# Performance work log

Hardware: AMD Instinct MI355X
Metric: run time of the kernel (lower is better)

The kernel has to match this reference:

```python
import math
import jax, jax.numpy as jnp
import numpy as np

T, D, H, HD, ETA, R = 4096, 1024, 8, 64, 4, 7
EPS = 1e-5


def _discounted_sum(start_state, x, discounts):
    """state[t] = state[t-1]*discounts[t] + x[t], scanned over leading axis T."""
    def step(s, xd):
        xt, dt = xd
        s = s * dt + xt
        return s, s
    _, ys = jax.lax.scan(step, start_state, (x, discounts))
    return ys  # (T, *)


def _forward(inputs, terminations, tilde_k_prev, tilde_v_prev, s_prev, tick,
             W_kqv, b_kqv, W_p, b_p, W_proj, b_proj):
    cur_seq = inputs.shape[0]
    term = terminations.astype(inputs.dtype)

    kqv = (inputs @ W_kqv + b_kqv).reshape(cur_seq, H, 5 * HD)
    keys, queries, values, beta, gammas = jnp.split(kqv, 5, axis=-1)  # each (T,H,HD)
    p = (inputs @ W_p + b_p).reshape(cur_seq, H, 3 * ETA)
    p1, p2, p3 = jnp.split(p, 3, axis=-1)  # each (T,H,ETA)

    # feature-map expansion: outer product over (eta, head_dim) -> flatten to eta*HD
    keys = jnp.einsum('chd,chn->chnd', jax.nn.relu(keys), jax.nn.relu(p1)).reshape(cur_seq, H, ETA * HD)
    queries = jnp.einsum('chd,chn->chnd', jax.nn.relu(queries), jax.nn.relu(p2)).reshape(cur_seq, H, ETA * HD)
    gammas = jnp.einsum('chd,chn->chnd', jax.nn.sigmoid(gammas), jax.nn.sigmoid(p3)).reshape(cur_seq, H, ETA * HD)
    beta = jax.nn.sigmoid(beta)  # (T,H,HD)

    ticks = tick.reshape(1, 1) + jnp.arange(1, cur_seq + 1, dtype=inputs.dtype).reshape(-1, 1)  # (T,1)->(T,R)
    omegas = jnp.linspace(-math.pi, math.pi, R).astype(inputs.dtype).reshape(1, -1)
    occil = jnp.cos(ticks * omegas)  # (T,R)

    values = values * beta
    values = values[:, None, :, :] * occil[:, :, None, None]  # (T,R,H,HD)
    keys = keys * gammas
    s = keys  # (T,H,ETA*HD)
    keys = keys[:, None, :, :] * occil[:, :, None, None]  # (T,R,H,ETA*HD)

    not_term = (1.0 - term).reshape(cur_seq, 1, 1)
    discount_gamma = (1.0 - gammas) * not_term  # (T,H,ETA*HD)
    discount_beta = (1.0 - beta) * not_term     # (T,H,HD)

    final_keys = _discounted_sum(tilde_k_prev, keys, discount_gamma[:, None])    # (T,R,H,ETA*HD)
    final_values = _discounted_sum(tilde_v_prev, values, discount_beta[:, None])  # (T,R,H,HD)
    final_s = _discounted_sum(s_prev, s, discount_gamma)                          # (T,H,ETA*HD)

    kdq = jnp.einsum('crhd,chd->crh', final_keys, queries)
    kv = jnp.einsum('crhd,crh->chd', final_values, kdq)  # sum over r
    norm = jnp.einsum('chd,chd->ch', final_s, queries)
    attn_out = kv / (2 * R * norm[..., None] + EPS)
    attn_out = attn_out.reshape(cur_seq, H * HD) @ W_proj + b_proj  # dropout p=0.0 is identity

    new_tick = tick + cur_seq
    return attn_out, final_keys[-1], final_values[-1], final_s[-1], new_tick


def setup_inputs() -> dict:
    key = jax.random.key(0)
    ks = jax.random.split(key, 5)
    return {
        'inputs': jax.random.normal(ks[0], (T, D), jnp.float32),
        'terminations': jax.random.randint(ks[1], (T,), 0, 2, jnp.int32),
        'tilde_k_prev': jnp.zeros((R, H, ETA * HD), jnp.float32),
        'tilde_v_prev': jnp.zeros((R, H, HD), jnp.float32),
        's_prev': jnp.zeros((H, ETA * HD), jnp.float32),
        'tick': jnp.ones((1,), jnp.float32),
        'W_kqv': jax.random.normal(ks[2], (D, H * HD * 5), jnp.float32) * 0.02,
        'b_kqv': jnp.zeros((H * HD * 5,), jnp.float32),
        'W_p': jax.random.normal(ks[3], (D, H * ETA * 3), jnp.float32) * 0.02,
        'b_p': jnp.zeros((H * ETA * 3,), jnp.float32),
        'W_proj': jax.random.normal(ks[4], (H * HD, D), jnp.float32) * 0.02,
        'b_proj': jnp.zeros((D,), jnp.float32),
    }


def reference(inputs, terminations, tilde_k_prev, tilde_v_prev, s_prev, tick,
              W_kqv, b_kqv, W_p, b_p, W_proj, b_proj):
    return _forward(inputs, terminations, tilde_k_prev, tilde_v_prev, s_prev, tick,
                    W_kqv, b_kqv, W_p, b_p, W_proj, b_proj)
```

## Files before the change

### kernel.cpp

```cpp
#include <hip/hip_runtime.h>
#include <hip/hip_bf16.h>
#include <math.h>

#define T_SEQ 4096
#define DIM   1024
#define NH    8
#define HDIM  64
#define ETA   4
#define NR    7
#define NKQVC 2688
#define CHUNK 16
#define NCHUNK 256

typedef __attribute__((ext_vector_type(8))) short bf16x8;
typedef __attribute__((ext_vector_type(4))) short short4v;
typedef __attribute__((ext_vector_type(4))) float f32x4;

#define KQVC_OFF    0ul
#define OCC_OFF     5505024ul
#define BTPROJ_OFF  5537792ul
#define ATTNBF_OFF  5799936ul
#define BIASC_OFF   6848512ul
#define ABF_OFF     6851328ul
#define BTCAT_OFF   8948480ul
#define YSUM_OFF    6851328ul
#define GBUF_OFF    12618496ul

#define O_ATTN 0ul
#define O_FK   4194304ul
#define O_FV   4208640ul
#define O_FS   4212224ul
#define O_TICK 4214272ul

__device__ __forceinline__ float sigm(float x) { return 1.f / (1.f + __expf(-x)); }

__device__ __forceinline__ short f2bf(float f) {
  union { __hip_bfloat16 b; short s; } u;
  u.b = __float2bfloat16(f);
  return u.s;
}
__device__ __forceinline__ float bf2f(short s) {
  union { __hip_bfloat16 b; short s2; } u;
  u.s2 = s;
  return __bfloat162float(u.b);
}

__device__ __forceinline__ void gload16(const void* g, void* l) {
  __builtin_amdgcn_global_load_lds(
      (const __attribute__((address_space(1))) void*)g,
      (__attribute__((address_space(3))) void*)l, 16, 0, 0);
}

__global__ __launch_bounds__(256) void cast_f32_bf16(
    const float* __restrict__ x, short* __restrict__ y) {
  size_t i = (size_t)(blockIdx.x * 256 + threadIdx.x) * 4;
  float4 v = *(const float4*)(x + i);
  short4v o;
  o.x = f2bf(v.x); o.y = f2bf(v.y); o.z = f2bf(v.z); o.w = f2bf(v.w);
  *(short4v*)(y + i) = o;
}

__global__ __launch_bounds__(256) void transpose_cast(
    const float* __restrict__ W, short* __restrict__ Bt, int K, int N) {
  __shared__ float tile[32][33];
  int n0 = blockIdx.x * 32, k0 = blockIdx.y * 32;
  int tx = threadIdx.x, ty = threadIdx.y;
  for (int i = ty; i < 32; i += 8)
    tile[i][tx] = W[(size_t)(k0 + i) * N + n0 + tx];
  __syncthreads();
  for (int i = ty; i < 32; i += 8)
    Bt[(size_t)(n0 + i) * K + k0 + tx] = f2bf(tile[tx][i]);
}

__global__ __launch_bounds__(256) void concat_bias(
    const float* __restrict__ b_kqv, const float* __restrict__ b_p,
    float* __restrict__ bc) {
  int i = blockIdx.x * 256 + threadIdx.x;
  if (i >= NKQVC) return;
  bc[i] = (i < 2560) ? b_kqv[i] : (i < 2656 ? b_p[i - 2560] : 0.f);
}

template <int OUT_BF16>
__global__ __launch_bounds__(256) void gemm_bt_mfma(
    const short* __restrict__ A, const short* __restrict__ Bt,
    const float* __restrict__ bias, void* __restrict__ Cout,
    int M, int N, int K) {
  __shared__ __align__(16) short lds[16384];

  int nwg = gridDim.x;
  int cpx = nwg >> 3;
  int bid = blockIdx.x;
  int swz = (bid & 7) * cpx + (bid >> 3);
  int nbx = N >> 7;
  int bm0 = (swz / nbx) << 7;
  int bn0 = (swz % nbx) << 7;

  const int tid = threadIdx.x;
  const int w = tid >> 6, l = tid & 63;
  const int wm = w >> 1, wn = w & 1;
  const int fr = l & 15;
  const int fq = l >> 4;

  const int ca = w * 2;
  const short* Ag0 = A + (size_t)(bm0 + ca * 16 + (l >> 2)) * K + (l & 3) * 8;
  const short* Ag1 = Ag0 + (size_t)16 * K;
  const short* Bg0 = Bt + (size_t)(bn0 + ca * 16 + (l >> 2)) * K + (l & 3) * 8;
  const short* Bg1 = Bg0 + (size_t)16 * K;

  f32x4 acc[4][4];
#pragma unroll
  for (int mi = 0; mi < 4; ++mi)
#pragma unroll
    for (int ni = 0; ni < 4; ++ni)
#pragma unroll
      for (int r = 0; r < 4; ++r) acc[mi][ni][r] = 0.f;

  const int KT = K >> 5;
  int cur = 0;
  {
    short* la = &lds[ca * 512];
    short* lb = &lds[4096 + ca * 512];
    gload16(Ag0, la);
    gload16(Ag1, la + 512);
    gload16(Bg0, lb);
    gload16(Bg1, lb + 512);
  }
  __syncthreads();

  for (int kt = 0; kt < KT; ++kt) {
    if (kt + 1 < KT) {
      int nb = (cur ^ 1) * 8192;
      int ko = (kt + 1) * 32;
      short* la = &lds[nb + ca * 512];
      short* lb = &lds[nb + 4096 + ca * 512];
      gload16(Ag0 + ko, la);
      gload16(Ag1 + ko, la + 512);
      gload16(Bg0 + ko, lb);
      gload16(Bg1 + ko, lb + 512);
    }
    const short* ArP = &lds[cur * 8192 + (wm * 64 + fr) * 32 + fq * 8];
    const short* BrP = &lds[cur * 8192 + 4096 + (wn * 64 + fr) * 32 + fq * 8];
    bf16x8 af[4], bfv[4];
#pragma unroll
    for (int mi = 0; mi < 4; ++mi) af[mi] = *(const bf16x8*)(ArP + mi * 512);
#pragma unroll
    for (int ni = 0; ni < 4; ++ni) bfv[ni] = *(const bf16x8*)(BrP + ni * 512);
#pragma unroll
    for (int mi = 0; mi < 4; ++mi)
#pragma unroll
      for (int ni = 0; ni < 4; ++ni)
        acc[mi][ni] = __builtin_amdgcn_mfma_f32_16x16x32_bf16(
            af[mi], bfv[ni], acc[mi][ni], 0, 0, 0);
    __syncthreads();
    cur ^= 1;
  }

  if (OUT_BF16) {
#pragma unroll
    for (int ni = 0; ni < 4; ++ni) {
      int col = wn * 64 + ni * 16 + fr;
      float bz = bias[bn0 + col];
#pragma unroll
      for (int mi = 0; mi < 4; ++mi) {
        int row = wm * 64 + mi * 16 + fq * 4;
#pragma unroll
        for (int r = 0; r < 4; ++r)
          lds[(row + r) * 128 + col] = f2bf(acc[mi][ni][r] + bz);
      }
    }
    __syncthreads();
    int row = tid >> 1, half = tid & 1;
    const f32x4* src = (const f32x4*)&lds[row * 128 + half * 64];
    f32x4* dst = (f32x4*)((short*)Cout + (size_t)(bm0 + row) * N + bn0 + half * 64);
#pragma unroll
    for (int i = 0; i < 8; ++i) dst[i] = src[i];
  } else {
#pragma unroll
    for (int ni = 0; ni < 4; ++ni) {
      int col = bn0 + wn * 64 + ni * 16 + fr;
      float bz = bias[col];
#pragma unroll
      for (int mi = 0; mi < 4; ++mi) {
        int row = bm0 + wm * 64 + mi * 16 + fq * 4;
#pragma unroll
        for (int r = 0; r < 4; ++r)
          ((float*)Cout)[(size_t)(row + r) * N + col] = acc[mi][ni][r] + bz;
      }
    }
  }
}

__global__ __launch_bounds__(256) void occil_kernel(const float* __restrict__ tick,
                                                    float* __restrict__ occ) {
  int t = blockIdx.x * 256 + threadIdx.x;
  if (t >= T_SEQ) return;
  float tickt = tick[0] + (float)(t + 1);
#pragma unroll
  for (int r = 0; r < NR; ++r) {
    float om = (float)(-3.14159265358979323846 + r * (3.14159265358979323846 / 3.0));
    occ[t * 8 + r] = cosf(tickt * om);
  }
  occ[t * 8 + 7] = 0.f;
}

__global__ __launch_bounds__(256) void gates_kernel(
    const short* __restrict__ kqv, const int* __restrict__ term,
    short* __restrict__ gbuf) {
  int u = blockIdx.x * 4 + (threadIdx.x >> 6);
  int dd = threadIdx.x & 63;
  int t = u >> 3, h = u & 7;
  size_t base = (size_t)t * NKQVC + h * 320 + dd;
  float kx = bf2f(kqv[base]);
  float qx = bf2f(kqv[base + 64]);
  float vx = bf2f(kqv[base + 128]);
  float bx = bf2f(kqv[base + 192]);
  float gx = bf2f(kqv[base + 256]);
  const short* pp = kqv + (size_t)t * NKQVC + 2560 + h * 12;
  float nt = 1.f - (float)term[t];
  float rk = fmaxf(kx, 0.f), rq = fmaxf(qx, 0.f);
  float sg = sigm(gx), sb = sigm(bx);
  bf16x8 oA, oB;
#pragma unroll
  for (int n = 0; n < 4; ++n) {
    float rp1 = fmaxf(bf2f(pp[n]), 0.f);
    float rp2 = fmaxf(bf2f(pp[4 + n]), 0.f);
    float sp3 = sigm(bf2f(pp[8 + n]));
    float gam = sg * sp3;
    oA[n]     = f2bf(rk * rp1 * gam);
    oA[4 + n] = f2bf((1.f - gam) * nt);
    oB[n]     = f2bf(rq * rp2);
  }
  oB[4] = f2bf(vx * sb);
  oB[5] = f2bf((1.f - sb) * nt);
  oB[6] = 0; oB[7] = 0;
  short* dst = gbuf + ((size_t)u * 64 + dd) * 16;
  *(bf16x8*)dst = oA;
  *(bf16x8*)(dst + 8) = oB;
}

__global__ __launch_bounds__(256) void pass_a(
    const short* __restrict__ gbuf, const float* __restrict__ occ,
    float* __restrict__ ysum) {
  const int c = blockIdx.x, h = blockIdx.y;
  const int tid = threadIdx.x;
  const int w = tid >> 6, dd = tid & 63;
  const int R0 = w * 2;
  const int RN = (w == 3) ? 1 : 2;
  const bool w3 = (w == 3);
  __shared__ float socc[CHUNK][8];
  for (int i = tid; i < CHUNK * 8; i += 256)
    socc[i >> 3][i & 7] = occ[(size_t)c * CHUNK * 8 + i];
  __syncthreads();

  float yk[2][ETA], yv[2], ys[ETA], Pg[ETA], Pb = 1.f;
#pragma unroll
  for (int rr = 0; rr < 2; ++rr) {
    yv[rr] = 0.f;
#pragma unroll
    for (int n = 0; n < ETA; ++n) yk[rr][n] = 0.f;
  }
#pragma unroll
  for (int n = 0; n < ETA; ++n) { ys[n] = 0.f; Pg[n] = 1.f; }

  const size_t TSTR = (size_t)8 * 64 * 16;
  const short* gb = gbuf + (((size_t)(c * CHUNK) * 8 + h) * 64 + dd) * 16;
  bf16x8 gA = *(const bf16x8*)gb;
  bf16x8 gB = *(const bf16x8*)(gb + 8);
  for (int t = 0; t < CHUNK; ++t) {
    const short* gn = gb + (t < CHUNK - 1 ? TSTR : 0);
    bf16x8 nA = *(const bf16x8*)gn;
    bf16x8 nB = *(const bf16x8*)(gn + 8);

    float occr[2];
#pragma unroll
    for (int rr = 0; rr < 2; ++rr)
      occr[rr] = socc[t][(R0 + rr) < 7 ? (R0 + rr) : 7];
#pragma unroll
    for (int n = 0; n < ETA; ++n) {
      float xs = bf2f(gA[n]);
      float dg = bf2f(gA[4 + n]);
      if (w3) {
        Pg[n] *= dg;
        ys[n] = fmaf(ys[n], dg, xs);
      }
#pragma unroll
      for (int rr = 0; rr < 2; ++rr)
        if (rr < RN) yk[rr][n] = fmaf(yk[rr][n], dg, xs * occr[rr]);
    }
    float vb = bf2f(gB[4]);
    float db = bf2f(gB[5]);
    if (w3) Pb *= db;
#pragma unroll
    for (int rr = 0; rr < 2; ++rr)
      if (rr < RN) yv[rr] = fmaf(yv[rr], db, vb * occr[rr]);

    gA = nA; gB = nB; gb = gn;
  }

  float* o = ysum + (size_t)(c * NH + h) * 44 * 64 + dd;
#pragma unroll
  for (int rr = 0; rr < 2; ++rr)
    if (rr < RN) {
#pragma unroll
      for (int n = 0; n < ETA; ++n) o[((R0 + rr) * 4 + n) * 64] = yk[rr][n];
      o[(28 + R0 + rr) * 64] = yv[rr];
    }
  if (w3) {
#pragma unroll
    for (int n = 0; n < ETA; ++n) o[(35 + n) * 64] = ys[n];
#pragma unroll
    for (int n = 0; n < ETA; ++n) o[(39 + n) * 64] = Pg[n];
    o[43 * 64] = Pb;
  }
}

__global__ __launch_bounds__(256) void pass_b(
    float* __restrict__ ysum, const float* __restrict__ k_prev,
    const float* __restrict__ v_prev, const float* __restrict__ s_prev) {
  int idx = blockIdx.x * 256 + threadIdx.x;
  int dd = idx & 63;
  int slot = (idx >> 6) % 39;
  int h = idx / (39 * 64);

  int pslot;
  float f;
  if (slot < 28) {
    int r = slot >> 2, n = slot & 3;
    f = k_prev[(size_t)(r * NH + h) * 256 + n * 64 + dd];
    pslot = 39 + n;
  } else if (slot < 35) {
    int r = slot - 28;
    f = v_prev[(size_t)(r * NH + h) * 64 + dd];
    pslot = 43;
  } else {
    int n = slot - 35;
    f = s_prev[(size_t)h * 256 + n * 64 + dd];
    pslot = 39 + n;
  }
  const size_t STRIDE = (size_t)NH * 2816;
  float* yb = ysum + (size_t)h * 2816 + slot * 64 + dd;
  const float* pb = ysum + (size_t)h * 2816 + pslot * 64 + dd;

#define PD 16
  float yring[PD], pring[PD];
#pragma unroll
  for (int d = 0; d < PD; ++d) {
    yring[d] = yb[(size_t)d * STRIDE];
    pring[d] = pb[(size_t)d * STRIDE];
  }
  const int NB = NCHUNK / PD;
  for (int cb = 0; cb < NB; ++cb) {
    int c0 = cb * PD;
    float ynext[PD], pnext[PD];
    if (cb + 1 < NB) {
#pragma unroll
      for (int j = 0; j < PD; ++j) {
        ynext[j] = yb[(size_t)(c0 + PD + j) * STRIDE];
        pnext[j] = pb[(size_t)(c0 + PD + j) * STRIDE];
      }
    }
#pragma unroll
    for (int j = 0; j < PD; ++j) {
      yb[(size_t)(c0 + j) * STRIDE] = f;
      f = fmaf(f, pring[j], yring[j]);
    }
    if (cb + 1 < NB) {
#pragma unroll
      for (int j = 0; j < PD; ++j) { yring[j] = ynext[j]; pring[j] = pnext[j]; }
    }
  }
#undef PD
}

__global__ __launch_bounds__(256) void pass_c(
    const short* __restrict__ gbuf, const float* __restrict__ occ,
    const float* __restrict__ carry, short* __restrict__ attn,
    float* __restrict__ out, const float* __restrict__ tick) {
  const int c = blockIdx.x, h = blockIdx.y;
  const int tid = threadIdx.x;
  const int w = tid >> 6, dd = tid & 63;
  const int R0 = w * 2;
  const int RN = (w == 3) ? 1 : 2;
  const bool w3 = (w == 3);
  __shared__ float socc[CHUNK][8];
  __shared__ float xch[5][CHUNK][64];
  for (int i = tid; i < CHUNK * 8; i += 256)
    socc[i >> 3][i & 7] = occ[(size_t)c * CHUNK * 8 + i];

  const float* cp = carry + (size_t)(c * NH + h) * 2816 + dd;
  float fk[2][ETA], fv[2], fs[ETA];
#pragma unroll
  for (int rr = 0; rr < 2; ++rr)
    if (rr < RN) {
#pragma unroll
      for (int n = 0; n < ETA; ++n) fk[rr][n] = cp[((R0 + rr) * 4 + n) * 64];
      fv[rr] = cp[(28 + R0 + rr) * 64];
    }
  if (w3) {
#pragma unroll
    for (int n = 0; n < ETA; ++n) fs[n] = cp[(35 + n) * 64];
  }
  __syncthreads();

  const size_t TSTR = (size_t)8 * 64 * 16;
  const short* gb = gbuf + (((size_t)(c * CHUNK) * 8 + h) * 64 + dd) * 16;
  bf16x8 gA = *(const bf16x8*)gb;
  bf16x8 gB = *(const bf16x8*)(gb + 8);
  for (int t = 0; t < CHUNK; ++t) {
    const short* gn = gb + (t < CHUNK - 1 ? TSTR : 0);
    bf16x8 nA = *(const bf16x8*)gn;
    bf16x8 nB = *(const bf16x8*)(gn + 8);

    float occr[2];
#pragma unroll
    for (int rr = 0; rr < 2; ++rr)
      occr[rr] = socc[t][(R0 + rr) < 7 ? (R0 + rr) : 7];
    float kdqp[2] = {0.f, 0.f};
    float normp = 0.f;
#pragma unroll
    for (int n = 0; n < ETA; ++n) {
      float xs = bf2f(gA[n]);
      float dg = bf2f(gA[4 + n]);
      float qf = bf2f(gB[n]);
      if (w3) {
        fs[n] = fmaf(fs[n], dg, xs);
        normp = fmaf(fs[n], qf, normp);
      }
#pragma unroll
      for (int rr = 0; rr < 2; ++rr)
        if (rr < RN) {
          fk[rr][n] = fmaf(fk[rr][n], dg, xs * occr[rr]);
          kdqp[rr]  = fmaf(fk[rr][n], qf, kdqp[rr]);
        }
    }
    float vb = bf2f(gB[4]);
    float db = bf2f(gB[5]);
#pragma unroll
    for (int rr = 0; rr < 2; ++rr)
      if (rr < RN) fv[rr] = fmaf(fv[rr], db, vb * occr[rr]);

    float red[2];
    red[0] = kdqp[0];
    red[1] = w3 ? normp : kdqp[1];
#pragma unroll
    for (int i = 0; i < 2; ++i) {
      float x = red[i];
#pragma unroll
      for (int m = 1; m < 64; m <<= 1) x += __shfl_xor(x, m, 64);
      red[i] = x;
    }
    float kvvP = fv[0] * red[0];
    if (!w3) kvvP = fmaf(fv[1], red[1], kvvP);
    xch[w][t][dd] = kvvP;
    if (w3) xch[4][t][dd] = fmaf(14.f, red[1], 1e-5f);

    gA = nA; gB = nB; gb = gn;
  }
  __syncthreads();

#pragma unroll
  for (int j = 0; j < 4; ++j) {
    int t = w * 4 + j;
    float kvv = xch[0][t][dd] + xch[1][t][dd] + xch[2][t][dd] + xch[3][t][dd];
    attn[(size_t)(c * CHUNK + t) * 512 + h * 64 + dd] = f2bf(kvv / xch[4][t][dd]);
  }

  if (c == NCHUNK - 1) {
#pragma unroll
    for (int rr = 0; rr < 2; ++rr)
      if (rr < RN) {
#pragma unroll
        for (int n = 0; n < ETA; ++n)
          out[O_FK + (size_t)((R0 + rr) * NH + h) * 256 + n * 64 + dd] = fk[rr][n];
        out[O_FV + (size_t)((R0 + rr) * NH + h) * 64 + dd] = fv[rr];
      }
    if (w3) {
#pragma unroll
      for (int n = 0; n < ETA; ++n)
        out[O_FS + (size_t)h * 256 + n * 64 + dd] = fs[n];
    }
    if (w == 0 && h == 0 && dd == 0) out[O_TICK] = tick[0] + (float)T_SEQ;
  }
}

extern "C" void kernel_launch(void* const* d_in, const int* in_sizes, int n_in,
                              void* d_out, int out_size, void* d_ws, size_t ws_size,
                              hipStream_t stream) {
  const float* inputs = (const float*)d_in[0];
  const int*   term   = (const int*)d_in[1];
  const float* k_prev = (const float*)d_in[2];
  const float* v_prev = (const float*)d_in[3];
  const float* s_prev = (const float*)d_in[4];
  const float* tick   = (const float*)d_in[5];
  const float* W_kqv  = (const float*)d_in[6];
  const float* b_kqv  = (const float*)d_in[7];
  const float* W_p    = (const float*)d_in[8];
  const float* b_p    = (const float*)d_in[9];
  const float* W_proj = (const float*)d_in[10];
  const float* b_proj = (const float*)d_in[11];
  float* out = (float*)d_out;
  float* ws  = (float*)d_ws;

  short* kqvc   = (short*)(ws + KQVC_OFF);
  float* occ    = ws + OCC_OFF;
  short* BtProj = (short*)(ws + BTPROJ_OFF);
  short* attnbf = (short*)(ws + ATTNBF_OFF);
  float* biasc  = ws + BIASC_OFF;
  short* Abf    = (short*)(ws + ABF_OFF);
  short* BtCat  = (short*)(ws + BTCAT_OFF);
  float* ysum   = ws + YSUM_OFF;
  short* gbuf   = (short*)(ws + GBUF_OFF);

  cast_f32_bf16<<<4096, 256, 0, stream>>>(inputs, Abf);
  transpose_cast<<<dim3(80, 32), dim3(32, 8), 0, stream>>>(W_kqv, BtCat, 1024, 2560);
  transpose_cast<<<dim3(3, 32), dim3(32, 8), 0, stream>>>(
      W_p, BtCat + (size_t)2560 * 1024, 1024, 96);
  transpose_cast<<<dim3(32, 16), dim3(32, 8), 0, stream>>>(W_proj, BtProj, 512, 1024);
  concat_bias<<<11, 256, 0, stream>>>(b_kqv, b_p, biasc);

  occil_kernel<<<16, 256, 0, stream>>>(tick, occ);

  gemm_bt_mfma<1><<<672, 256, 0, stream>>>(Abf, BtCat, biasc, kqvc,
                                           T_SEQ, NKQVC, DIM);

  gates_kernel<<<8192, 256, 0, stream>>>(kqvc, term, gbuf);

  pass_a<<<dim3(NCHUNK, NH), 256, 0, stream>>>(gbuf, occ, ysum);
  pass_b<<<78, 256, 0, stream>>>(ysum, k_prev, v_prev, s_prev);
  pass_c<<<dim3(NCHUNK, NH), 256, 0, stream>>>(gbuf, occ, ysum,
                                               attnbf, out, tick);

  gemm_bt_mfma<0><<<256, 256, 0, stream>>>(attnbf, BtProj, b_proj, out,
                                           T_SEQ, DIM, NH * HDIM);
}
```

Measured before the change: 156.0 us.

## Fuse gate computation into scan passes via shared-memory staging

Removes the standalone gates kernel and its global gbuf buffer. Pass A and pass C now each compute the gated features for their chunk and head directly from the kqv GEMM output and stage them in LDS. This saves one launch plus a write and two reads of the gate buffer, at the cost of computing the gates twice (once per pass) and using 32KB of extra LDS per block, which may lower occupancy.

```diff
diff --git a/kernel.cpp b/kernel.cpp
--- a/kernel.cpp
+++ b/kernel.cpp
@@ -24,7 +24,6 @@
 #define ABF_OFF     6851328ul
 #define BTCAT_OFF   8948480ul
 #define YSUM_OFF    6851328ul
-#define GBUF_OFF    12618496ul
 
 #define O_ATTN 0ul
 #define O_FK   4194304ul
@@ -203,53 +202,56 @@
   occ[t * 8 + 7] = 0.f;
 }
 
-__global__ __launch_bounds__(256) void gates_kernel(
+__device__ __forceinline__ void stage_gates(
     const short* __restrict__ kqv, const int* __restrict__ term,
-    short* __restrict__ gbuf) {
-  int u = blockIdx.x * 4 + (threadIdx.x >> 6);
-  int dd = threadIdx.x & 63;
-  int t = u >> 3, h = u & 7;
-  size_t base = (size_t)t * NKQVC + h * 320 + dd;
-  float kx = bf2f(kqv[base]);
-  float qx = bf2f(kqv[base + 64]);
-  float vx = bf2f(kqv[base + 128]);
-  float bx = bf2f(kqv[base + 192]);
-  float gx = bf2f(kqv[base + 256]);
-  const short* pp = kqv + (size_t)t * NKQVC + 2560 + h * 12;
-  float nt = 1.f - (float)term[t];
-  float rk = fmaxf(kx, 0.f), rq = fmaxf(qx, 0.f);
-  float sg = sigm(gx), sb = sigm(bx);
-  bf16x8 oA, oB;
-#pragma unroll
-  for (int n = 0; n < 4; ++n) {
-    float rp1 = fmaxf(bf2f(pp[n]), 0.f);
-    float rp2 = fmaxf(bf2f(pp[4 + n]), 0.f);
-    float sp3 = sigm(bf2f(pp[8 + n]));
-    float gam = sg * sp3;
-    oA[n]     = f2bf(rk * rp1 * gam);
-    oA[4 + n] = f2bf((1.f - gam) * nt);
-    oB[n]     = f2bf(rq * rp2);
-  }
-  oB[4] = f2bf(vx * sb);
-  oB[5] = f2bf((1.f - sb) * nt);
-  oB[6] = 0; oB[7] = 0;
-  short* dst = gbuf + ((size_t)u * 64 + dd) * 16;
-  *(bf16x8*)dst = oA;
-  *(bf16x8*)(dst + 8) = oB;
+    short* glds, int c, int h, int w, int dd) {
+#pragma unroll
+  for (int j = 0; j < 4; ++j) {
+    int t = w * 4 + j;
+    int tg = c * CHUNK + t;
+    size_t base = (size_t)tg * NKQVC + h * 320 + dd;
+    float kx = bf2f(kqv[base]);
+    float qx = bf2f(kqv[base + 64]);
+    float vx = bf2f(kqv[base + 128]);
+    float bx = bf2f(kqv[base + 192]);
+    float gx = bf2f(kqv[base + 256]);
+    const short* pp = kqv + (size_t)tg * NKQVC + 2560 + h * 12;
+    float nt = 1.f - (float)term[tg];
+    float rk = fmaxf(kx, 0.f), rq = fmaxf(qx, 0.f);
+    float sg = sigm(gx), sb = sigm(bx);
+    bf16x8 oA, oB;
+#pragma unroll
+    for (int n = 0; n < 4; ++n) {
+      float rp1 = fmaxf(bf2f(pp[n]), 0.f);
+      float rp2 = fmaxf(bf2f(pp[4 + n]), 0.f);
+      float sp3 = sigm(bf2f(pp[8 + n]));
+      float gam = sg * sp3;
+      oA[n]     = f2bf(rk * rp1 * gam);
+      oA[4 + n] = f2bf((1.f - gam) * nt);
+      oB[n]     = f2bf(rq * rp2);
+    }
+    oB[4] = f2bf(vx * sb);
+    oB[5] = f2bf((1.f - sb) * nt);
+    oB[6] = 0; oB[7] = 0;
+    *(bf16x8*)&glds[(t * 64 + dd) * 16] = oA;
+    *(bf16x8*)&glds[(t * 64 + dd) * 16 + 8] = oB;
+  }
 }
 
 __global__ __launch_bounds__(256) void pass_a(
-    const short* __restrict__ gbuf, const float* __restrict__ occ,
-    float* __restrict__ ysum) {
+    const short* __restrict__ kqv, const float* __restrict__ occ,
+    const int* __restrict__ term, float* __restrict__ ysum) {
   const int c = blockIdx.x, h = blockIdx.y;
   const int tid = threadIdx.x;
   const int w = tid >> 6, dd = tid & 63;
   const int R0 = w * 2;
   const int RN = (w == 3) ? 1 : 2;
   const bool w3 = (w == 3);
+  __shared__ __align__(16) short glds[CHUNK * 64 * 16];
   __shared__ float socc[CHUNK][8];
   for (int i = tid; i < CHUNK * 8; i += 256)
     socc[i >> 3][i & 7] = occ[(size_t)c * CHUNK * 8 + i];
+  stage_gates(kqv, term, glds, c, h, w, dd);
   __syncthreads();
 
   float yk[2][ETA], yv[2], ys[ETA], Pg[ETA], Pb = 1.f;
@@ -262,15 +264,9 @@
 #pragma unroll
   for (int n = 0; n < ETA; ++n) { ys[n] = 0.f; Pg[n] = 1.f; }
 
-  const size_t TSTR = (size_t)8 * 64 * 16;
-  const short* gb = gbuf + (((size_t)(c * CHUNK) * 8 + h) * 64 + dd) * 16;
-  bf16x8 gA = *(const bf16x8*)gb;
-  bf16x8 gB = *(const bf16x8*)(gb + 8);
   for (int t = 0; t < CHUNK; ++t) {
-    const short* gn = gb + (t < CHUNK - 1 ? TSTR : 0);
-    bf16x8 nA = *(const bf16x8*)gn;
-    bf16x8 nB = *(const bf16x8*)(gn + 8);
-
+    bf16x8 gA = *(const bf16x8*)&glds[(t * 64 + dd) * 16];
+    bf16x8 gB = *(const bf16x8*)&glds[(t * 64 + dd) * 16 + 8];
     float occr[2];
 #pragma unroll
     for (int rr = 0; rr < 2; ++rr)
@@ -293,8 +289,6 @@
 #pragma unroll
     for (int rr = 0; rr < 2; ++rr)
       if (rr < RN) yv[rr] = fmaf(yv[rr], db, vb * occr[rr]);
-
-    gA = nA; gB = nB; gb = gn;
   }
 
   float* o = ysum + (size_t)(c * NH + h) * 44 * 64 + dd;
@@ -373,19 +367,22 @@
 }
 
 __global__ __launch_bounds__(256) void pass_c(
-    const short* __restrict__ gbuf, const float* __restrict__ occ,
-    const float* __restrict__ carry, short* __restrict__ attn,
-    float* __restrict__ out, const float* __restrict__ tick) {
+    const short* __restrict__ kqv, const float* __restrict__ occ,
+    const int* __restrict__ term, const float* __restrict__ carry,
+    short* __restrict__ attn, float* __restrict__ out,
+    const float* __restrict__ tick) {
   const int c = blockIdx.x, h = blockIdx.y;
   const int tid = threadIdx.x;
   const int w = tid >> 6, dd = tid & 63;
   const int R0 = w * 2;
   const int RN = (w == 3) ? 1 : 2;
   const bool w3 = (w == 3);
+  __shared__ __align__(16) short glds[CHUNK * 64 * 16];
   __shared__ float socc[CHUNK][8];
   __shared__ float xch[5][CHUNK][64];
   for (int i = tid; i < CHUNK * 8; i += 256)
     socc[i >> 3][i & 7] = occ[(size_t)c * CHUNK * 8 + i];
+  stage_gates(kqv, term, glds, c, h, w, dd);
 
   const float* cp = carry + (size_t)(c * NH + h) * 2816 + dd;
   float fk[2][ETA], fv[2], fs[ETA];
@@ -402,15 +399,9 @@
   }
   __syncthreads();
 
-  const size_t TSTR = (size_t)8 * 64 * 16;
-  const short* gb = gbuf + (((size_t)(c * CHUNK) * 8 + h) * 64 + dd) * 16;
-  bf16x8 gA = *(const bf16x8*)gb;
-  bf16x8 gB = *(const bf16x8*)(gb + 8);
   for (int t = 0; t < CHUNK; ++t) {
-    const short* gn = gb + (t < CHUNK - 1 ? TSTR : 0);
-    bf16x8 nA = *(const bf16x8*)gn;
-    bf16x8 nB = *(const bf16x8*)(gn + 8);
-
+    bf16x8 gA = *(const bf16x8*)&glds[(t * 64 + dd) * 16];
+    bf16x8 gB = *(const bf16x8*)&glds[(t * 64 + dd) * 16 + 8];
     float occr[2];
 #pragma unroll
     for (int rr = 0; rr < 2; ++rr)
@@ -453,8 +444,6 @@
     if (!w3) kvvP = fmaf(fv[1], red[1], kvvP);
     xch[w][t][dd] = kvvP;
     if (w3) xch[4][t][dd] = fmaf(14.f, red[1], 1e-5f);
-
-    gA = nA; gB = nB; gb = gn;
   }
   __syncthreads();
 
@@ -509,7 +498,6 @@
   short* Abf    = (short*)(ws + ABF_OFF);
   short* BtCat  = (short*)(ws + BTCAT_OFF);
   float* ysum   = ws + YSUM_OFF;
-  short* gbuf   = (short*)(ws + GBUF_OFF);
 
   cast_f32_bf16<<<4096, 256, 0, stream>>>(inputs, Abf);
   transpose_cast<<<dim3(80, 32), dim3(32, 8), 0, stream>>>(W_kqv, BtCat, 1024, 2560);
@@ -523,11 +511,9 @@
   gemm_bt_mfma<1><<<672, 256, 0, stream>>>(Abf, BtCat, biasc, kqvc,
                                            T_SEQ, NKQVC, DIM);
 
-  gates_kernel<<<8192, 256, 0, stream>>>(kqvc, term, gbuf);
-
-  pass_a<<<dim3(NCHUNK, NH), 256, 0, stream>>>(gbuf, occ, ysum);
+  pass_a<<<dim3(NCHUNK, NH), 256, 0, stream>>>(kqvc, occ, term, ysum);
   pass_b<<<78, 256, 0, stream>>>(ysum, k_prev, v_prev, s_prev);
-  pass_c<<<dim3(NCHUNK, NH), 256, 0, stream>>>(gbuf, occ, ysum,
+  pass_c<<<dim3(NCHUNK, NH), 256, 0, stream>>>(kqvc, occ, term, ysum,
                                                attnbf, out, tick);
 
   gemm_bt_mfma<0><<<256, 256, 0, stream>>>(attnbf, BtProj, b_proj, out,
```

Result: faster. 147.0 us (-5.8%).
